# Kernel tuning notes

Measured on AMD Instinct MI355X. Metric: run time of the kernel, lower is better.

Reference implementation:

```python
import jax, jax.numpy as jnp
import numpy as np

EPS = 1e-5
NUM_HEADS = 12

def _ln(x, g, b):
    m = jnp.mean(x, -1, keepdims=True)
    v = jnp.var(x, -1, keepdims=True)
    return (x - m) * jax.lax.rsqrt(v + EPS) * g + b

def setup_inputs():
    key = jax.random.key(0)
    ks = jax.random.split(key, 8)
    D, Dh = 768, 3072
    B, T, H, Wd = 8, 8, 14, 14
    def w(k, shape, scale=0.02):
        return jax.random.normal(k, shape, jnp.float32) * scale
    return dict(
        x=jax.random.normal(ks[0], (B, T * H * Wd + 1, D), jnp.float32),
        W_mq=w(ks[1], (D, D)), b_mq=jnp.zeros((D,), jnp.float32),
        W_mk=w(ks[2], (D, D)), b_mk=jnp.zeros((D,), jnp.float32),
        g1=jnp.ones((D,), jnp.float32), be1=jnp.zeros((D,), jnp.float32),
        W_qkv=w(ks[3], (3 * D, D)),
        W_proj=w(ks[4], (D, D)), b_proj=jnp.zeros((D,), jnp.float32),
        g2=jnp.ones((D,), jnp.float32), be2=jnp.zeros((D,), jnp.float32),
        W_fc1=w(ks[5], (Dh, D)), b_fc1=jnp.zeros((Dh,), jnp.float32),
        W_fc2=w(ks[6], (D, Dh)), b_fc2=jnp.zeros((D,), jnp.float32),
        B=B, T=T, H=H, Wd=Wd,
    )

def reference(x, W_mq, b_mq, W_mk, b_mk, g1, be1, W_qkv, W_proj, b_proj,
              g2, be2, W_fc1, b_fc1, W_fc2, b_fc2, B, T, H, Wd):
    D = x.shape[-1]
    nh = NUM_HEADS
    hd = D // nh
    res = x
    # cls token: (B,1,D) -> repeated per frame -> (B*T,1,D)
    cls = jnp.repeat(x[:, :1, :], T, axis=1).reshape(B * T, 1, D)
    # spatial tokens: 'b (h w t) m -> (b t) (h w) m'  (t is fastest-varying)
    xs = x[:, 1:, :].reshape(B, H * Wd, T, D).transpose(0, 2, 1, 3).reshape(B * T, H * Wd, D)
    xt = jnp.concatenate([cls, xs], axis=1)  # (BT, N=197, D)
    # learned QK-gated mask
    qm = xt @ W_mq.T + b_mq
    km = xt @ W_mk.T + b_mk
    lm = jnp.einsum('bnd,bmd->bnm', qm, km)
    lm = lm.at[:, 0, 0].set(100.0)  # force cls->cls gate open
    lm = jax.nn.sigmoid(lm)
    # attention (drop rates are 0; drop_path is identity at inference)
    xn = _ln(xt, g1, be1)
    BT, N = xt.shape[0], xt.shape[1]
    qkv = (xn @ W_qkv.T).reshape(BT, N, 3, nh, hd).transpose(2, 0, 3, 1, 4)
    q, k, v = qkv[0], qkv[1], qkv[2]  # (BT, nh, N, hd)
    attn = jax.nn.softmax(jnp.einsum('bhnd,bhmd->bhnm', q, k) * (hd ** -0.5), axis=-1)
    attn = attn * lm[:, None, :, :]  # gate attention probs with learned mask
    o = jnp.einsum('bhnm,bhmd->bhnd', attn, v).transpose(0, 2, 1, 3).reshape(BT, N, D)
    o = o @ W_proj.T + b_proj
    # gather cls back (mean over frames) and scatter tokens back
    cls_o = jnp.mean(o[:, 0, :].reshape(B, T, D), axis=1, keepdims=True)  # (B,1,D)
    xs_o = o[:, 1:, :].reshape(B, T, H * Wd, D).transpose(0, 2, 1, 3).reshape(B, H * Wd * T, D)
    y = res + jnp.concatenate([cls_o, xs_o], axis=1)
    # MLP
    h = _ln(y, g2, be2)
    h = jax.nn.gelu(h @ W_fc1.T + b_fc1, approximate=False)
    y = y + (h @ W_fc2.T + b_fc2)
    return (y, lm)
```

## Files before the change

### kernel.cpp

```cpp
#include <hip/hip_runtime.h>
#include <cstdint>

typedef _Float16 f16;
typedef f16 f16x2 __attribute__((ext_vector_type(2)));
typedef f16 f16x4 __attribute__((ext_vector_type(4)));
typedef f16 f16x8 __attribute__((ext_vector_type(8)));
typedef float f32x4 __attribute__((ext_vector_type(4)));

constexpr int D = 768;
constexpr int NTOK = 197;
constexpr int BT = 64;
constexpr int ROWS_A = BT * NTOK;
constexpr int SEQ = 1569;
constexpr int ROWS_Y = 8 * SEQ;
constexpr int DH = 3072;
constexpr int CW = 2304;
constexpr long Y_ELEMS = (long)ROWS_Y * D;
constexpr long LM_ELEMS = (long)BT * NTOK * NTOK;

__device__ __forceinline__ void gload_lds16(const f16* g, f16* l) {
  __builtin_amdgcn_global_load_lds(
      (const __attribute__((address_space(1))) void*)g,
      (__attribute__((address_space(3))) void*)l, 16, 0, 0);
}

__global__ __launch_bounds__(256) void cvt_f16(const float* __restrict__ in,
                                               f16* __restrict__ out, int n4) {
  int i = blockIdx.x * 256 + threadIdx.x;
  if (i >= n4) return;
  const float4 v = *(const float4*)(in + (size_t)i * 4);
  f16x4 o = {(f16)v.x, (f16)v.y, (f16)v.z, (f16)v.w};
  *(f16x4*)(out + (size_t)i * 4) = o;
}

__global__ __launch_bounds__(192) void build_xt_xn(
    const float* __restrict__ x, const float* __restrict__ g1,
    const float* __restrict__ be1, f16* __restrict__ xt, f16* __restrict__ xn) {
  const int rid = blockIdx.x;
  const int bt = rid / NTOK, n = rid % NTOK;
  const int b = bt >> 3, t = bt & 7;
  const int src = (n == 0) ? b * SEQ : b * SEQ + 1 + (n - 1) * 8 + t;
  const int tid = threadIdx.x, d0 = tid * 4;
  const float4 v = *(const float4*)(x + (size_t)src * D + d0);
  float s = v.x + v.y + v.z + v.w;
  float q = v.x * v.x + v.y * v.y + v.z * v.z + v.w * v.w;
  const int lane = tid & 63, wv = tid >> 6;
  for (int off = 32; off; off >>= 1) {
    s += __shfl_xor(s, off);
    q += __shfl_xor(q, off);
  }
  __shared__ float red[2][3];
  if (lane == 0) { red[0][wv] = s; red[1][wv] = q; }
  __syncthreads();
  s = red[0][0] + red[0][1] + red[0][2];
  q = red[1][0] + red[1][1] + red[1][2];
  const float mean = s * (1.f / 768.f);
  const float var = q * (1.f / 768.f) - mean * mean;
  const float rs = rsqrtf(var + 1e-5f);
  const size_t ob = (size_t)rid * D + d0;
  f16x4 xo = {(f16)v.x, (f16)v.y, (f16)v.z, (f16)v.w};
  *(f16x4*)(xt + ob) = xo;
  const float4 gv = *(const float4*)(g1 + d0);
  const float4 bv = *(const float4*)(be1 + d0);
  f16x4 no = {(f16)((v.x - mean) * rs * gv.x + bv.x),
              (f16)((v.y - mean) * rs * gv.y + bv.y),
              (f16)((v.z - mean) * rs * gv.z + bv.z),
              (f16)((v.w - mean) * rs * gv.w + bv.w)};
  *(f16x4*)(xn + ob) = no;
}

constexpr int EPI_F16 = 0;
constexpr int EPI_F16_BIAS = 1;
constexpr int EPI_SIG = 2;
constexpr int EPI_F16_BIAS_GELU = 3;
constexpr int EPI_F32_BIAS_RES = 4;

template <int EPI>
__global__ __launch_bounds__(256, 3) void gemm_f16(
    const f16* __restrict__ A, const f16* __restrict__ B,
    const float* __restrict__ bias, float* __restrict__ Cf,
    f16* __restrict__ Ch, const float* __restrict__ Res, int M, int N, int K,
    int ldc, long sA, long sB, long sC) {
  constexpr int BM = 128, BN = 128, BK = 64;
  __shared__ f16 As[BM][BK];
  __shared__ f16 Bs[BN][BK];
  const int tid = threadIdx.x;
  const int bm = blockIdx.y * BM, bn = blockIdx.x * BN;
  const int z = blockIdx.z;
  A += (size_t)z * sA;
  B += (size_t)z * sB;
  const int lane = tid & 63, wave = tid >> 6;
  const int wm = (wave >> 1) * 64, wn = (wave & 1) * 64;
  const int l15 = lane & 15, quad = lane >> 4;

  const int gr = lane >> 3;
  const int gc = (lane & 7) * 8;
  const f16* apg[4];
  const f16* bpg[4];
  f16* asd[4];
  f16* bsd[4];
#pragma unroll
  for (int g = 0; g < 4; g++) {
    int ar = bm + (wave + 4 * g) * 8 + gr;  if (ar >= M) ar = M - 1;
    int br = bn + (wave + 4 * g) * 8 + gr;  if (br >= N) br = N - 1;
    apg[g] = A + (size_t)ar * K + gc;
    bpg[g] = B + (size_t)br * K + gc;
    asd[g] = &As[(wave + 4 * g) * 8][0];
    bsd[g] = &Bs[(wave + 4 * g) * 8][0];
  }

  f32x4 acc[4][4] = {};

  for (int kt = 0; kt < K; kt += BK) {
#pragma unroll
    for (int g = 0; g < 4; g++) {
      gload_lds16(apg[g] + kt, asd[g]);
      gload_lds16(bpg[g] + kt, bsd[g]);
    }
    __syncthreads();
#pragma unroll
    for (int ks = 0; ks < BK; ks += 32) {
      f16x8 af[4], bf[4];
#pragma unroll
      for (int i = 0; i < 4; i++) {
        af[i] = *(const f16x8*)&As[wm + i * 16 + l15][ks + quad * 8];
        bf[i] = *(const f16x8*)&Bs[wn + i * 16 + l15][ks + quad * 8];
      }
#pragma unroll
      for (int i = 0; i < 4; i++)
#pragma unroll
        for (int j = 0; j < 4; j++)
          acc[i][j] = __builtin_amdgcn_mfma_f32_16x16x32_f16(af[i], bf[j],
                                                             acc[i][j], 0, 0, 0);
    }
    __syncthreads();
  }

#pragma unroll
  for (int i = 0; i < 4; i++) {
#pragma unroll
    for (int j = 0; j < 4; j++) {
      const int col = bn + wn + j * 16 + l15;
      if (col >= N) continue;
#pragma unroll
      for (int r = 0; r < 4; r++) {
        const int row = bm + wm + i * 16 + quad * 4 + r;
        if (row >= M) continue;
        float v = acc[i][j][r];
        const size_t ci = (size_t)z * sC + (size_t)row * ldc + col;
        if constexpr (EPI == EPI_F16) {
          Ch[ci] = (f16)v;
        } else if constexpr (EPI == EPI_F16_BIAS) {
          Ch[ci] = (f16)(v + bias[col]);
        } else if constexpr (EPI == EPI_SIG) {
          if (row == 0 && col == 0) v = 100.f;
          Cf[ci] = 1.f / (1.f + __expf(-v));
        } else if constexpr (EPI == EPI_F16_BIAS_GELU) {
          const float u = v + bias[col];
          const float t = u * (0.79788456f + 0.0356774081f * u * u);
          const float e = __expf(2.f * t);
          Ch[ci] = (f16)(u * (e / (e + 1.f)));
        } else if constexpr (EPI == EPI_F32_BIAS_RES) {
          Cf[ci] = v + bias[col] + Res[ci];
        }
      }
    }
  }
}

__global__ __launch_bounds__(256, 2) void attn_kernel(
    const f16* __restrict__ qkv, const float* __restrict__ lm,
    f16* __restrict__ o) {
  __shared__ f16 Ks[208][72];
  __shared__ f16 Vt[64][232];
  __shared__ f16 Ps[4][16][40];
  const int bh = blockIdx.x;
  const int bt = bh / 12, h = bh % 12;
  const int tid = threadIdx.x, lane = tid & 63, w = tid >> 6;
  const int l15 = lane & 15, quad = lane >> 4;
  const size_t base = (size_t)bt * NTOK * CW + (size_t)h * 64;

  for (int idx = tid; idx < 208 * 8; idx += 256) {
    const int r = idx >> 3, c = (idx & 7) * 8;
    f16x8 kv = {};
    if (r < NTOK) kv = *(const f16x8*)(qkv + base + (size_t)r * CW + 768 + c);
    *(f16x8*)&Ks[r][c] = kv;
  }
  for (int cb = 0; cb < 8; cb++) {
    const int r = tid;
    if (r < NTOK) {
      const f16x8 vv = *(const f16x8*)(qkv + base + (size_t)r * CW + 1536 + cb * 8);
#pragma unroll
      for (int j = 0; j < 8; j++) Vt[cb * 8 + j][r] = vv[j];
    }
  }
  for (int idx = tid; idx < 64 * 35; idx += 256) {
    const int d = idx / 35, m = NTOK + idx % 35;
    Vt[d][m] = (f16)0.f;
  }
  __syncthreads();

  for (int nt = w; nt < 13; nt += 4) {
    const int nq = nt * 16 + l15;
    const f16* qrow = qkv + base + (size_t)nq * CW;
    const f16x8 aq0 = *(const f16x8*)(qrow + quad * 8);
    const f16x8 aq1 = *(const f16x8*)(qrow + 32 + quad * 8);
    f32x4 S[13];
#pragma unroll
    for (int t = 0; t < 13; t++) {
      const f16x8 bk0 = *(const f16x8*)&Ks[t * 16 + l15][quad * 8];
      const f16x8 bk1 = *(const f16x8*)&Ks[t * 16 + l15][32 + quad * 8];
      f32x4 s = {};
      s = __builtin_amdgcn_mfma_f32_16x16x32_f16(aq0, bk0, s, 0, 0, 0);
      s = __builtin_amdgcn_mfma_f32_16x16x32_f16(aq1, bk1, s, 0, 0, 0);
      S[t] = s;
    }
    float mx[4] = {-3e38f, -3e38f, -3e38f, -3e38f};
#pragma unroll
    for (int t = 0; t < 13; t++) {
      const int m = t * 16 + l15;
#pragma unroll
      for (int r = 0; r < 4; r++) {
        float v = (m < NTOK) ? S[t][r] * 0.125f : -1e30f;
        S[t][r] = v;
        mx[r] = fmaxf(mx[r], v);
      }
    }
#pragma unroll
    for (int off = 1; off < 16; off <<= 1)
#pragma unroll
      for (int r = 0; r < 4; r++) mx[r] = fmaxf(mx[r], __shfl_xor(mx[r], off));
    float den[4] = {0.f, 0.f, 0.f, 0.f};
#pragma unroll
    for (int t = 0; t < 13; t++)
#pragma unroll
      for (int r = 0; r < 4; r++) {
        const float e = __expf(S[t][r] - mx[r]);
        S[t][r] = e;
        den[r] += e;
      }
#pragma unroll
    for (int off = 1; off < 16; off <<= 1)
#pragma unroll
      for (int r = 0; r < 4; r++) den[r] += __shfl_xor(den[r], off);
    float inv[4];
#pragma unroll
    for (int r = 0; r < 4; r++) inv[r] = 1.f / den[r];
#pragma unroll
    for (int t = 0; t < 13; t++) {
      const int m = t * 16 + l15;
#pragma unroll
      for (int r = 0; r < 4; r++) {
        const int nrow = nt * 16 + quad * 4 + r;
        float g = 0.f;
        if (m < NTOK && nrow < NTOK)
          g = lm[((size_t)bt * NTOK + nrow) * NTOK + m];
        S[t][r] *= inv[r] * g;
      }
    }
    f32x4 O[4] = {};
    for (int c = 0; c < 7; c++) {
      __builtin_amdgcn_wave_barrier();
#pragma unroll
      for (int tt = 0; tt < 2; tt++) {
        const int t = 2 * c + tt;
#pragma unroll
        for (int r = 0; r < 4; r++) {
          const f16 pv = (t < 13) ? (f16)S[t][r] : (f16)0.f;
          Ps[w][quad * 4 + r][tt * 16 + l15] = pv;
        }
      }
      __builtin_amdgcn_wave_barrier();
      const f16x8 ap = *(const f16x8*)&Ps[w][l15][quad * 8];
#pragma unroll
      for (int dt = 0; dt < 4; dt++) {
        const f16x8 bv = *(const f16x8*)&Vt[dt * 16 + l15][c * 32 + quad * 8];
        O[dt] = __builtin_amdgcn_mfma_f32_16x16x32_f16(ap, bv, O[dt], 0, 0, 0);
      }
    }
#pragma unroll
    for (int dt = 0; dt < 4; dt++)
#pragma unroll
      for (int r = 0; r < 4; r++) {
        const int nrow = nt * 16 + quad * 4 + r;
        if (nrow < NTOK)
          o[((size_t)bt * NTOK + nrow) * D + h * 64 + dt * 16 + l15] =
              (f16)O[dt][r];
      }
  }
}

__global__ __launch_bounds__(192) void scatter_y_ln(
    const float* __restrict__ x, const f16* __restrict__ po,
    const float* __restrict__ g2, const float* __restrict__ be2,
    float* __restrict__ y, f16* __restrict__ yn) {
  const int rid = blockIdx.x;
  const int b = rid / SEQ, pos = rid % SEQ;
  const int tid = threadIdx.x, d0 = tid * 4;
  float4 v = *(const float4*)(x + (size_t)rid * D + d0);
  if (pos == 0) {
    float ax = 0, ay = 0, az = 0, aw = 0;
    for (int t = 0; t < 8; t++) {
      const f16x4 p = *(const f16x4*)(po + ((size_t)(b * 8 + t) * NTOK) * D + d0);
      ax += (float)p[0]; ay += (float)p[1]; az += (float)p[2]; aw += (float)p[3];
    }
    v.x += ax * 0.125f; v.y += ay * 0.125f; v.z += az * 0.125f; v.w += aw * 0.125f;
  } else {
    const int hw = (pos - 1) >> 3, t = (pos - 1) & 7;
    const f16x4 p =
        *(const f16x4*)(po + ((size_t)((b * 8 + t) * NTOK + 1 + hw)) * D + d0);
    v.x += (float)p[0]; v.y += (float)p[1]; v.z += (float)p[2]; v.w += (float)p[3];
  }
  *(float4*)(y + (size_t)rid * D + d0) = v;
  float s = v.x + v.y + v.z + v.w;
  float q = v.x * v.x + v.y * v.y + v.z * v.z + v.w * v.w;
  const int lane = tid & 63, wv = tid >> 6;
  for (int off = 32; off; off >>= 1) {
    s += __shfl_xor(s, off);
    q += __shfl_xor(q, off);
  }
  __shared__ float red[2][3];
  if (lane == 0) { red[0][wv] = s; red[1][wv] = q; }
  __syncthreads();
  s = red[0][0] + red[0][1] + red[0][2];
  q = red[1][0] + red[1][1] + red[1][2];
  const float mean = s * (1.f / 768.f);
  const float var = q * (1.f / 768.f) - mean * mean;
  const float rs = rsqrtf(var + 1e-5f);
  const float4 gv = *(const float4*)(g2 + d0);
  const float4 bv = *(const float4*)(be2 + d0);
  f16x4 no = {(f16)((v.x - mean) * rs * gv.x + bv.x),
              (f16)((v.y - mean) * rs * gv.y + bv.y),
              (f16)((v.z - mean) * rs * gv.z + bv.z),
              (f16)((v.w - mean) * rs * gv.w + bv.w)};
  *(f16x4*)(yn + (size_t)rid * D + d0) = no;
}

extern "C" void kernel_launch(void* const* d_in, const int* in_sizes, int n_in,
                              void* d_out, int out_size, void* d_ws,
                              size_t ws_size, hipStream_t stream) {
  const float* x = (const float*)d_in[0];
  const float* W_mq = (const float*)d_in[1];
  const float* b_mq = (const float*)d_in[2];
  const float* W_mk = (const float*)d_in[3];
  const float* b_mk = (const float*)d_in[4];
  const float* g1 = (const float*)d_in[5];
  const float* be1 = (const float*)d_in[6];
  const float* W_qkv = (const float*)d_in[7];
  const float* W_proj = (const float*)d_in[8];
  const float* b_proj = (const float*)d_in[9];
  const float* g2 = (const float*)d_in[10];
  const float* be2 = (const float*)d_in[11];
  const float* W_fc1 = (const float*)d_in[12];
  const float* b_fc1 = (const float*)d_in[13];
  const float* W_fc2 = (const float*)d_in[14];
  const float* b_fc2 = (const float*)d_in[15];

  char* ws = (char*)d_ws;
  size_t off = 0;
  auto alloc = [&](size_t bytes) {
    size_t o = off;
    off = (off + bytes + 255) & ~(size_t)255;
    return o;
  };
  const size_t o_wmq = alloc((size_t)D * D * 2);
  const size_t o_wmk = alloc((size_t)D * D * 2);
  const size_t o_wqkv = alloc((size_t)CW * D * 2);
  const size_t o_wproj = alloc((size_t)D * D * 2);
  const size_t o_wfc1 = alloc((size_t)DH * D * 2);
  const size_t o_wfc2 = alloc((size_t)D * DH * 2);
  const size_t o_xt = alloc((size_t)ROWS_A * D * 2);
  const size_t o_xn = alloc((size_t)ROWS_A * D * 2);
  const size_t o_qm = alloc((size_t)ROWS_A * D * 2);
  alloc((size_t)ROWS_A * D * 2);
  const size_t o_km = o_qm + (size_t)ROWS_A * D * 2;
  const size_t o_qkv = o_qm;
  const size_t o_o = o_xn;
  const size_t o_po = o_qm + (size_t)ROWS_A * CW * 2;
  const size_t o_yn = o_xt;
  const size_t o_h = o_qm;

  f16* wmq = (f16*)(ws + o_wmq);
  f16* wmk = (f16*)(ws + o_wmk);
  f16* wqkv = (f16*)(ws + o_wqkv);
  f16* wproj = (f16*)(ws + o_wproj);
  f16* wfc1 = (f16*)(ws + o_wfc1);
  f16* wfc2 = (f16*)(ws + o_wfc2);
  f16* xt = (f16*)(ws + o_xt);
  f16* xn = (f16*)(ws + o_xn);
  f16* qm = (f16*)(ws + o_qm);
  f16* km = (f16*)(ws + o_km);
  f16* qkv = (f16*)(ws + o_qkv);
  f16* oatt = (f16*)(ws + o_o);
  f16* po = (f16*)(ws + o_po);
  f16* yn = (f16*)(ws + o_yn);
  f16* h = (f16*)(ws + o_h);

  float* y_out = (float*)d_out;
  float* lm_out = (float*)d_out + Y_ELEMS;

  const dim3 blk(256);
  auto cvt = [&](const float* src, f16* dst, int n) {
    cvt_f16<<<dim3((n / 4 + 255) / 256), blk, 0, stream>>>(src, dst, n / 4);
  };
  cvt(W_mq, wmq, D * D);
  cvt(W_mk, wmk, D * D);
  cvt(W_qkv, wqkv, CW * D);
  cvt(W_proj, wproj, D * D);
  cvt(W_fc1, wfc1, DH * D);
  cvt(W_fc2, wfc2, D * DH);

  build_xt_xn<<<dim3(ROWS_A), dim3(192), 0, stream>>>(x, g1, be1, xt, xn);

  auto grd = [](int N_, int M_, int Z_) {
    return dim3((N_ + 127) / 128, (M_ + 127) / 128, Z_);
  };
  gemm_f16<EPI_F16_BIAS><<<grd(D, ROWS_A, 1), blk, 0, stream>>>(
      xt, wmq, b_mq, nullptr, qm, nullptr, ROWS_A, D, D, D, 0, 0, 0);
  gemm_f16<EPI_F16_BIAS><<<grd(D, ROWS_A, 1), blk, 0, stream>>>(
      xt, wmk, b_mk, nullptr, km, nullptr, ROWS_A, D, D, D, 0, 0, 0);
  gemm_f16<EPI_SIG><<<grd(NTOK, NTOK, BT), blk, 0, stream>>>(
      qm, km, nullptr, lm_out, nullptr, nullptr, NTOK, NTOK, D, NTOK,
      (long)NTOK * D, (long)NTOK * D, (long)NTOK * NTOK);
  gemm_f16<EPI_F16><<<grd(CW, ROWS_A, 1), blk, 0, stream>>>(
      xn, wqkv, nullptr, nullptr, qkv, nullptr, ROWS_A, CW, D, CW, 0, 0, 0);
  attn_kernel<<<dim3(BT * 12), blk, 0, stream>>>(qkv, lm_out, oatt);
  gemm_f16<EPI_F16_BIAS><<<grd(D, ROWS_A, 1), blk, 0, stream>>>(
      oatt, wproj, b_proj, nullptr, po, nullptr, ROWS_A, D, D, D, 0, 0, 0);
  scatter_y_ln<<<dim3(ROWS_Y), dim3(192), 0, stream>>>(x, po, g2, be2, y_out, yn);
  gemm_f16<EPI_F16_BIAS_GELU><<<grd(DH, ROWS_Y, 1), blk, 0, stream>>>(
      yn, wfc1, b_fc1, nullptr, h, nullptr, ROWS_Y, DH, D, DH, 0, 0, 0);
  gemm_f16<EPI_F32_BIAS_RES><<<grd(D, ROWS_Y, 1), blk, 0, stream>>>(
      h, wfc2, b_fc2, y_out, nullptr, y_out, ROWS_Y, D, DH, D, 0, 0, 0);
  (void)in_sizes; (void)n_in; (void)out_size; (void)ws_size;
}
```

Before: 684.9 us.

## Replace LDS-staged GEMM tiles with direct register loads and double buffering

The GEMM kernel no longer stages A and B tiles through shared memory with global_load_lds and barriers. Each wave now loads its MFMA operand fragments straight from global memory into registers, with two register buffers so the next k-slice is in flight while the current one computes. Launch bounds drop from 3 to 2 blocks per CU to make room for the extra registers. This removes the LDS traffic and syncthreads, but each wave reloads data its neighbours also read, so global/L2 traffic goes up and the loads are strided per lane rather than coalesced.

```diff
diff --git a/kernel.cpp b/kernel.cpp
--- a/kernel.cpp
+++ b/kernel.cpp
@@ -17,12 +17,6 @@
 constexpr int CW = 2304;
 constexpr long Y_ELEMS = (long)ROWS_Y * D;
 constexpr long LM_ELEMS = (long)BT * NTOK * NTOK;
-
-__device__ __forceinline__ void gload_lds16(const f16* g, f16* l) {
-  __builtin_amdgcn_global_load_lds(
-      (const __attribute__((address_space(1))) void*)g,
-      (__attribute__((address_space(3))) void*)l, 16, 0, 0);
-}
 
 __global__ __launch_bounds__(256) void cvt_f16(const float* __restrict__ in,
                                                f16* __restrict__ out, int n4) {
@@ -76,14 +70,12 @@
 constexpr int EPI_F32_BIAS_RES = 4;
 
 template <int EPI>
-__global__ __launch_bounds__(256, 3) void gemm_f16(
+__global__ __launch_bounds__(256, 2) void gemm_f16(
     const f16* __restrict__ A, const f16* __restrict__ B,
     const float* __restrict__ bias, float* __restrict__ Cf,
     f16* __restrict__ Ch, const float* __restrict__ Res, int M, int N, int K,
     int ldc, long sA, long sB, long sC) {
-  constexpr int BM = 128, BN = 128, BK = 64;
-  __shared__ f16 As[BM][BK];
-  __shared__ f16 Bs[BN][BK];
+  constexpr int BM = 128, BN = 128;
   const int tid = threadIdx.x;
   const int bm = blockIdx.y * BM, bn = blockIdx.x * BN;
   const int z = blockIdx.z;
@@ -93,47 +85,47 @@
   const int wm = (wave >> 1) * 64, wn = (wave & 1) * 64;
   const int l15 = lane & 15, quad = lane >> 4;
 
-  const int gr = lane >> 3;
-  const int gc = (lane & 7) * 8;
-  const f16* apg[4];
-  const f16* bpg[4];
-  f16* asd[4];
-  f16* bsd[4];
-#pragma unroll
-  for (int g = 0; g < 4; g++) {
-    int ar = bm + (wave + 4 * g) * 8 + gr;  if (ar >= M) ar = M - 1;
-    int br = bn + (wave + 4 * g) * 8 + gr;  if (br >= N) br = N - 1;
-    apg[g] = A + (size_t)ar * K + gc;
-    bpg[g] = B + (size_t)br * K + gc;
-    asd[g] = &As[(wave + 4 * g) * 8][0];
-    bsd[g] = &Bs[(wave + 4 * g) * 8][0];
+  unsigned oA[4], oB[4];
+#pragma unroll
+  for (int i = 0; i < 4; i++) {
+    int ra = bm + wm + i * 16 + l15; if (ra >= M) ra = M - 1;
+    int cb = bn + wn + i * 16 + l15; if (cb >= N) cb = N - 1;
+    oA[i] = (unsigned)ra * (unsigned)K + quad * 8;
+    oB[i] = (unsigned)cb * (unsigned)K + quad * 8;
   }
 
   f32x4 acc[4][4] = {};
-
-  for (int kt = 0; kt < K; kt += BK) {
-#pragma unroll
-    for (int g = 0; g < 4; g++) {
-      gload_lds16(apg[g] + kt, asd[g]);
-      gload_lds16(bpg[g] + kt, bsd[g]);
-    }
-    __syncthreads();
-#pragma unroll
-    for (int ks = 0; ks < BK; ks += 32) {
-      f16x8 af[4], bf[4];
+  f16x8 a0[4], b0[4], a1[4], b1[4];
+#pragma unroll
+  for (int i = 0; i < 4; i++) {
+    a0[i] = *(const f16x8*)(A + oA[i]);
+    b0[i] = *(const f16x8*)(B + oB[i]);
+  }
+  for (int kt = 0; kt < K; kt += 64) {
+#pragma unroll
+    for (int i = 0; i < 4; i++) {
+      a1[i] = *(const f16x8*)(A + oA[i] + kt + 32);
+      b1[i] = *(const f16x8*)(B + oB[i] + kt + 32);
+    }
+#pragma unroll
+    for (int i = 0; i < 4; i++)
+#pragma unroll
+      for (int j = 0; j < 4; j++)
+        acc[i][j] =
+            __builtin_amdgcn_mfma_f32_16x16x32_f16(a0[i], b0[j], acc[i][j], 0, 0, 0);
+    if (kt + 64 < K) {
 #pragma unroll
       for (int i = 0; i < 4; i++) {
-        af[i] = *(const f16x8*)&As[wm + i * 16 + l15][ks + quad * 8];
-        bf[i] = *(const f16x8*)&Bs[wn + i * 16 + l15][ks + quad * 8];
-      }
-#pragma unroll
-      for (int i = 0; i < 4; i++)
-#pragma unroll
-        for (int j = 0; j < 4; j++)
-          acc[i][j] = __builtin_amdgcn_mfma_f32_16x16x32_f16(af[i], bf[j],
-                                                             acc[i][j], 0, 0, 0);
-    }
-    __syncthreads();
+        a0[i] = *(const f16x8*)(A + oA[i] + kt + 64);
+        b0[i] = *(const f16x8*)(B + oB[i] + kt + 64);
+      }
+    }
+#pragma unroll
+    for (int i = 0; i < 4; i++)
+#pragma unroll
+      for (int j = 0; j < 4; j++)
+        acc[i][j] =
+            __builtin_amdgcn_mfma_f32_16x16x32_f16(a1[i], b1[j], acc[i][j], 0, 0, 0);
   }
 
 #pragma unroll
```

Result: slower. 1.162 ms (+69.6%).
